# Performance work log

Hardware: AMD Instinct MI355X
Metric: run time of the kernel (lower is better)

## Reference

```python
import jax, jax.numpy as jnp
import numpy as np

TEMPERATURE = 0.5
NEG_FILL = -9000000000000000.0


def setup_inputs() -> dict:
    key = jax.random.key(0)
    z = jax.random.normal(key, (16384, 128), dtype=jnp.float32)
    return {"z": z}


def reference(z) -> jnp.ndarray:
    n2 = z.shape[0]  # 2N
    # L2 normalize rows (eps matches torch F.normalize default 1e-12)
    norm = jnp.maximum(jnp.linalg.norm(z, axis=1, keepdims=True), 1e-12)
    zn = z / norm
    # (2N, 2N) cosine similarity scaled by temperature
    sim = jnp.matmul(zn, zn.T) / TEMPERATURE
    # mask self-similarity on the diagonal
    idx = jnp.arange(n2)
    sim = jnp.where(idx[:, None] == idx[None, :], NEG_FILL, sim)
    # positive pair of row i is i^1 (2i <-> 2i+1)
    pos_indices = idx ^ 1
    pos_sim = sim[idx, pos_indices]
    loss = -pos_sim + jax.scipy.special.logsumexp(sim, axis=1)
    return jnp.mean(loss)
```

## Files before the change

### kernel.cpp

```cpp
#include <hip/hip_runtime.h>
#include <hip/hip_bf16.h>

#define N2 16384
#define D  128
#define PANEL 32768
#define C1   2.88539008177792681472f
#define SQC1 1.69864360258810896f
#define LN2  0.69314718055994530942f

typedef __bf16 bf16x8 __attribute__((ext_vector_type(8)));
typedef float  f32x4  __attribute__((ext_vector_type(4)));

#if __has_builtin(__builtin_amdgcn_exp2f)
#define EXP2(x) __builtin_amdgcn_exp2f(x)
#else
#define EXP2(x) exp2f(x)
#endif

__device__ __forceinline__ unsigned short f2bf(float f) {
    union { float f; unsigned u; } v; v.f = f;
    unsigned r = v.u + 0x7fffu + ((v.u >> 16) & 1u);
    return (unsigned short)(r >> 16);
}

__device__ __forceinline__ void stage_panel(const char* __restrict__ g,
                                            char* lds, int tid) {
    const int wid = tid >> 6, lane = tid & 63;
    #pragma unroll
    for (int i = 0; i < 8; ++i) {
        int off = (wid << 13) + (i << 10) + (lane << 4);
        int src = off ^ (((off >> 8) & 7) << 4);
        __builtin_amdgcn_global_load_lds(
            (const __attribute__((address_space(1))) unsigned*)(g + src),
            (__attribute__((address_space(3))) unsigned*)(lds + (wid << 13) + (i << 10)),
            16, 0, 0);
    }
}

__global__ void k_norm(const float* __restrict__ z, unsigned short* __restrict__ zn) {
    int row  = blockIdx.x * 4 + (threadIdx.x >> 6);
    int lane = threadIdx.x & 63;
    const float2 v = ((const float2*)(z + (size_t)row * D))[lane];
    float ss = v.x * v.x + v.y * v.y;
    #pragma unroll
    for (int m = 1; m < 64; m <<= 1) ss += __shfl_xor(ss, m);
    float inv = SQC1 / fmaxf(sqrtf(ss), 1e-12f);
    ushort2 o; o.x = f2bf(v.x * inv); o.y = f2bf(v.y * inv);
    ((ushort2*)(zn + (size_t)row * D))[lane] = o;
}

__global__ __launch_bounds__(256, 2)
void k_sim(const unsigned short* __restrict__ zn, float* __restrict__ rowsum) {
    __shared__ unsigned short ls[2][PANEL / 2];
    char* ls0 = (char*)&ls[0][0];
    char* ls1 = (char*)&ls[1][0];

    const int tileI = blockIdx.y;
    const int sBase = blockIdx.x * 16;
    const int nt = (blockIdx.x == 3 && tileI < 64) ? 17 : 16;
    const int tid  = threadIdx.x;
    const int lane = tid & 63, wid = tid >> 6;
    const int wr = wid >> 1, wc = wid & 1;
    const int l16 = lane & 15, lg = lane >> 4;
    const char* znb = (const char*)zn;
    const f32x4 ZERO = {0.f, 0.f, 0.f, 0.f};

    stage_panel(znb + (size_t)tileI * PANEL, ls0, tid);
    stage_panel(znb + (size_t)((tileI + sBase) & 127) * PANEL, ls1, tid);
    asm volatile("s_waitcnt vmcnt(8)" ::: "memory");
    __builtin_amdgcn_s_barrier();

    bf16x8 af[4][4];
    #pragma unroll
    for (int kk = 0; kk < 4; ++kk)
        #pragma unroll
        for (int m = 0; m < 4; ++m) {
            int row = wr * 64 + m * 16 + l16;
            int d = row * 256 + kk * 64 + lg * 16;
            af[kk][m] = *(const bf16x8*)(ls0 + (d ^ ((row & 7) << 4)));
        }
    asm volatile("s_waitcnt lgkmcnt(0)" ::: "memory");
    __builtin_amdgcn_s_barrier();

    float rs[4][4];
    #pragma unroll
    for (int m = 0; m < 4; ++m)
        #pragma unroll
        for (int r = 0; r < 4; ++r) rs[m][r] = 0.f;

    for (int t = 0; t < nt; ++t) {
        const int s  = sBase + t;
        const int jt = (tileI + s) & 127;
        char* rbuf = (t & 1) ? ls0 : ls1;
        char* sbuf = (t & 1) ? ls1 : ls0;
        if (t < nt - 1) {
            stage_panel(znb + (size_t)((tileI + s + 1) & 127) * PANEL, sbuf, tid);
            asm volatile("s_waitcnt vmcnt(8)" ::: "memory");
        } else {
            asm volatile("s_waitcnt vmcnt(0)" ::: "memory");
        }
        __builtin_amdgcn_s_barrier();

        bf16x8 bfr[4][4];
        #pragma unroll
        for (int kk = 0; kk < 4; ++kk)
            #pragma unroll
            for (int n = 0; n < 4; ++n) {
                int row = wc * 64 + n * 16 + l16;
                int d = row * 256 + kk * 64 + lg * 16;
                bfr[kk][n] = *(const bf16x8*)(rbuf + (d ^ ((row & 7) << 4)));
            }
        asm volatile("s_waitcnt lgkmcnt(0)" ::: "memory");
        __builtin_amdgcn_s_barrier();

        f32x4 acc[4][4];
        #pragma unroll
        for (int m = 0; m < 4; ++m)
            #pragma unroll
            for (int n = 0; n < 4; ++n)
                acc[m][n] = __builtin_amdgcn_mfma_f32_16x16x32_bf16(af[0][m], bfr[0][n], ZERO, 0, 0, 0);
        #pragma unroll
        for (int kk = 1; kk < 4; ++kk)
            #pragma unroll
            for (int m = 0; m < 4; ++m)
                #pragma unroll
                for (int n = 0; n < 4; ++n)
                    acc[m][n] = __builtin_amdgcn_mfma_f32_16x16x32_bf16(af[kk][m], bfr[kk][n], acc[m][n], 0, 0, 0);

        if (s == 0) {
            #pragma unroll
            for (int m = 0; m < 4; ++m)
                #pragma unroll
                for (int r = 0; r < 4; ++r) {
                    int li = wr * 64 + m * 16 + lg * 4 + r;
                    float a = 0.f;
                    #pragma unroll
                    for (int n = 0; n < 4; ++n) {
                        int lj = wc * 64 + n * 16 + l16;
                        float e = EXP2(acc[m][n][r]);
                        a += (li == lj) ? 0.f : e;
                    }
                    rs[m][r] += a;
                }
        } else {
            float cs[4] = {0.f, 0.f, 0.f, 0.f};
            #pragma unroll
            for (int m = 0; m < 4; ++m)
                #pragma unroll
                for (int r = 0; r < 4; ++r) {
                    float a = 0.f;
                    #pragma unroll
                    for (int n = 0; n < 4; ++n) {
                        float e = EXP2(acc[m][n][r]);
                        a += e;
                        cs[n] += e;
                    }
                    rs[m][r] += a;
                }
            #pragma unroll
            for (int n = 0; n < 4; ++n) {
                float v = cs[n];
                v += __shfl_xor(v, 16);
                v += __shfl_xor(v, 32);
                if (lg == 0)
                    atomicAdd(&rowsum[jt * 128 + wc * 64 + n * 16 + l16], v);
            }
        }
    }

    #pragma unroll
    for (int m = 0; m < 4; ++m)
        #pragma unroll
        for (int r = 0; r < 4; ++r) {
            float v = rs[m][r];
            v += __shfl_xor(v, 1);
            v += __shfl_xor(v, 2);
            v += __shfl_xor(v, 4);
            v += __shfl_xor(v, 8);
            if (l16 == 0)
                atomicAdd(&rowsum[tileI * 128 + wr * 64 + m * 16 + lg * 4 + r], v);
        }
}

__global__ void k_loss_reduce(const unsigned short* __restrict__ zn,
                              const float* __restrict__ rowsum,
                              float* __restrict__ out) {
    const int tid = threadIdx.x + blockIdx.x * 256;
    float p = 0.f;
    const bf16x8* v8 = (const bf16x8*)zn;
    for (int v = tid; v < N2 * D / 8; v += 64 * 256) {
        bf16x8 a = v8[v];
        bf16x8 b = v8[v ^ 16];
        #pragma unroll
        for (int e = 0; e < 8; ++e) p += (float)a[e] * (float)b[e];
    }
    float part = logf(rowsum[tid]) - LN2 * p;

    __shared__ float sm[4];
    #pragma unroll
    for (int m = 1; m < 64; m <<= 1) part += __shfl_xor(part, m);
    if ((threadIdx.x & 63) == 0) sm[threadIdx.x >> 6] = part;
    __syncthreads();
    if (threadIdx.x == 0)
        atomicAdd(out, (sm[0] + sm[1] + sm[2] + sm[3]) * (1.0f / (float)N2));
}

extern "C" void kernel_launch(void* const* d_in, const int* in_sizes, int n_in,
                              void* d_out, int out_size, void* d_ws, size_t ws_size,
                              hipStream_t stream) {
    const float* z = (const float*)d_in[0];
    float* out = (float*)d_out;

    unsigned short* zn = (unsigned short*)d_ws;
    float* rowsum = (float*)((char*)d_ws + (size_t)N2 * D * 2);

    hipMemsetAsync(rowsum, 0, N2 * sizeof(float), stream);
    hipMemsetAsync(out, 0, sizeof(float), stream);
    k_norm<<<N2 / 4, 256, 0, stream>>>(z, zn);
    dim3 grid(4, 128);
    k_sim<<<grid, 256, 0, stream>>>(zn, rowsum);
    k_loss_reduce<<<64, 256, 0, stream>>>(zn, rowsum, out);
}
```

Before: 68.50 us.

## Stream half-panels with smaller LDS, raise occupancy, fold memsets into norm kernel

The similarity kernel now stages half-panels of 64 rows into a 32KB LDS double buffer instead of full 128-row panels, which halves the B-fragment registers and accumulators per step. It raises launch bounds to three blocks per CU and widens the grid to six column chunks of 11 panel-steps, so more wavefronts can hide latency and the work spreads more evenly across CUs. The two memsets are removed and their zeroing moved into the normalization kernel, saving separate launches. The cost is twice as many barriers and pipeline steps per panel, more atomics per unit of work, and a serialized first panel load.

```diff
diff --git a/kernel.cpp b/kernel.cpp
--- a/kernel.cpp
+++ b/kernel.cpp
@@ -4,7 +4,7 @@
 #define N2 16384
 #define D  128
 #define PANEL 32768
-#define C1   2.88539008177792681472f
+#define HALFP 16384
 #define SQC1 1.69864360258810896f
 #define LN2  0.69314718055994530942f
 
@@ -37,7 +37,24 @@
     }
 }
 
-__global__ void k_norm(const float* __restrict__ z, unsigned short* __restrict__ zn) {
+__device__ __forceinline__ void stage_half(const char* __restrict__ g,
+                                           char* lds, int tid) {
+    const int wid = tid >> 6, lane = tid & 63;
+    #pragma unroll
+    for (int i = 0; i < 4; ++i) {
+        int off = (wid << 12) + (i << 10) + (lane << 4);
+        int src = off ^ (((off >> 8) & 7) << 4);
+        __builtin_amdgcn_global_load_lds(
+            (const __attribute__((address_space(1))) unsigned*)(g + src),
+            (__attribute__((address_space(3))) unsigned*)(lds + (wid << 12) + (i << 10)),
+            16, 0, 0);
+    }
+}
+
+__global__ void k_norm(const float* __restrict__ z, unsigned short* __restrict__ zn,
+                       float* __restrict__ rowsum, float* __restrict__ out) {
+    if (blockIdx.x < 64) rowsum[blockIdx.x * 256 + threadIdx.x] = 0.f;
+    if (blockIdx.x == 64 && threadIdx.x == 0) out[0] = 0.f;
     int row  = blockIdx.x * 4 + (threadIdx.x >> 6);
     int lane = threadIdx.x & 63;
     const float2 v = ((const float2*)(z + (size_t)row * D))[lane];
@@ -49,15 +66,17 @@
     ((ushort2*)(zn + (size_t)row * D))[lane] = o;
 }
 
-__global__ __launch_bounds__(256, 2)
+__global__ __launch_bounds__(256, 3)
 void k_sim(const unsigned short* __restrict__ zn, float* __restrict__ rowsum) {
-    __shared__ unsigned short ls[2][PANEL / 2];
-    char* ls0 = (char*)&ls[0][0];
-    char* ls1 = (char*)&ls[1][0];
-
+    __shared__ char ls[PANEL];
+    char* ls0 = ls;
+    char* ls1 = ls + HALFP;
     const int tileI = blockIdx.y;
-    const int sBase = blockIdx.x * 16;
-    const int nt = (blockIdx.x == 3 && tileI < 64) ? 17 : 16;
+    const int c = blockIdx.x;
+    const int sLo = c * 11;
+    const int sHi = (c < 5) ? (sLo + 11) : ((tileI < 64) ? 65 : 64);
+    const int Q = (sHi - sLo) * 2;
+
     const int tid  = threadIdx.x;
     const int lane = tid & 63, wid = tid >> 6;
     const int wr = wid >> 1, wc = wid & 1;
@@ -66,8 +85,7 @@
     const f32x4 ZERO = {0.f, 0.f, 0.f, 0.f};
 
     stage_panel(znb + (size_t)tileI * PANEL, ls0, tid);
-    stage_panel(znb + (size_t)((tileI + sBase) & 127) * PANEL, ls1, tid);
-    asm volatile("s_waitcnt vmcnt(8)" ::: "memory");
+    asm volatile("s_waitcnt vmcnt(0)" ::: "memory");
     __builtin_amdgcn_s_barrier();
 
     bf16x8 af[4][4];
@@ -82,49 +100,55 @@
     asm volatile("s_waitcnt lgkmcnt(0)" ::: "memory");
     __builtin_amdgcn_s_barrier();
 
+    stage_half(znb + (size_t)((tileI + sLo) & 127) * PANEL, ls0, tid);
+
     float rs[4][4];
     #pragma unroll
     for (int m = 0; m < 4; ++m)
         #pragma unroll
         for (int r = 0; r < 4; ++r) rs[m][r] = 0.f;
 
-    for (int t = 0; t < nt; ++t) {
-        const int s  = sBase + t;
+    for (int q = 0; q < Q; ++q) {
+        const int s  = sLo + (q >> 1);
+        const int h  = q & 1;
         const int jt = (tileI + s) & 127;
-        char* rbuf = (t & 1) ? ls0 : ls1;
-        char* sbuf = (t & 1) ? ls1 : ls0;
-        if (t < nt - 1) {
-            stage_panel(znb + (size_t)((tileI + s + 1) & 127) * PANEL, sbuf, tid);
-            asm volatile("s_waitcnt vmcnt(8)" ::: "memory");
+        char* rbuf = (q & 1) ? ls1 : ls0;
+        char* sbuf = (q & 1) ? ls0 : ls1;
+        if (q + 1 < Q) {
+            const int s1 = sLo + ((q + 1) >> 1);
+            const int h1 = (q + 1) & 1;
+            stage_half(znb + (size_t)((tileI + s1) & 127) * PANEL + h1 * HALFP,
+                       sbuf, tid);
+            asm volatile("s_waitcnt vmcnt(4)" ::: "memory");
         } else {
             asm volatile("s_waitcnt vmcnt(0)" ::: "memory");
         }
         __builtin_amdgcn_s_barrier();
 
-        bf16x8 bfr[4][4];
+        bf16x8 bfr[4][2];
         #pragma unroll
         for (int kk = 0; kk < 4; ++kk)
             #pragma unroll
-            for (int n = 0; n < 4; ++n) {
-                int row = wc * 64 + n * 16 + l16;
+            for (int n = 0; n < 2; ++n) {
+                int row = wc * 32 + n * 16 + l16;
                 int d = row * 256 + kk * 64 + lg * 16;
                 bfr[kk][n] = *(const bf16x8*)(rbuf + (d ^ ((row & 7) << 4)));
             }
         asm volatile("s_waitcnt lgkmcnt(0)" ::: "memory");
         __builtin_amdgcn_s_barrier();
 
-        f32x4 acc[4][4];
+        f32x4 acc[4][2];
         #pragma unroll
         for (int m = 0; m < 4; ++m)
             #pragma unroll
-            for (int n = 0; n < 4; ++n)
+            for (int n = 0; n < 2; ++n)
                 acc[m][n] = __builtin_amdgcn_mfma_f32_16x16x32_bf16(af[0][m], bfr[0][n], ZERO, 0, 0, 0);
         #pragma unroll
         for (int kk = 1; kk < 4; ++kk)
             #pragma unroll
             for (int m = 0; m < 4; ++m)
                 #pragma unroll
-                for (int n = 0; n < 4; ++n)
+                for (int n = 0; n < 2; ++n)
                     acc[m][n] = __builtin_amdgcn_mfma_f32_16x16x32_bf16(af[kk][m], bfr[kk][n], acc[m][n], 0, 0, 0);
 
         if (s == 0) {
@@ -135,35 +159,31 @@
                     int li = wr * 64 + m * 16 + lg * 4 + r;
                     float a = 0.f;
                     #pragma unroll
-                    for (int n = 0; n < 4; ++n) {
-                        int lj = wc * 64 + n * 16 + l16;
+                    for (int n = 0; n < 2; ++n) {
+                        int lj = h * 64 + wc * 32 + n * 16 + l16;
                         float e = EXP2(acc[m][n][r]);
                         a += (li == lj) ? 0.f : e;
                     }
                     rs[m][r] += a;
                 }
         } else {
-            float cs[4] = {0.f, 0.f, 0.f, 0.f};
+            float cs0 = 0.f, cs1 = 0.f;
             #pragma unroll
             for (int m = 0; m < 4; ++m)
                 #pragma unroll
                 for (int r = 0; r < 4; ++r) {
-                    float a = 0.f;
-                    #pragma unroll
-                    for (int n = 0; n < 4; ++n) {
-                        float e = EXP2(acc[m][n][r]);
-                        a += e;
-                        cs[n] += e;
-                    }
-                    rs[m][r] += a;
+                    float e0 = EXP2(acc[m][0][r]);
+                    float e1 = EXP2(acc[m][1][r]);
+                    rs[m][r] += e0 + e1;
+                    cs0 += e0; cs1 += e1;
                 }
-            #pragma unroll
-            for (int n = 0; n < 4; ++n) {
-                float v = cs[n];
-                v += __shfl_xor(v, 16);
-                v += __shfl_xor(v, 32);
-                if (lg == 0)
-                    atomicAdd(&rowsum[jt * 128 + wc * 64 + n * 16 + l16], v);
+            float v0 = cs0 + __shfl_xor(cs0, 16);
+            v0 += __shfl_xor(v0, 32);
+            float v1 = cs1 + __shfl_xor(cs1, 16);
+            v1 += __shfl_xor(v1, 32);
+            if (lg == 0) {
+                atomicAdd(&rowsum[jt * 128 + h * 64 + wc * 32 + l16], v0);
+                atomicAdd(&rowsum[jt * 128 + h * 64 + wc * 32 + 16 + l16], v1);
             }
         }
     }
@@ -214,10 +234,8 @@
     unsigned short* zn = (unsigned short*)d_ws;
     float* rowsum = (float*)((char*)d_ws + (size_t)N2 * D * 2);
 
-    hipMemsetAsync(rowsum, 0, N2 * sizeof(float), stream);
-    hipMemsetAsync(out, 0, sizeof(float), stream);
-    k_norm<<<N2 / 4, 256, 0, stream>>>(z, zn);
-    dim3 grid(4, 128);
+    k_norm<<<N2 / 4 , 256, 0, stream>>>(z, zn, rowsum, out);
+    dim3 grid(6, 128);
     k_sim<<<grid, 256, 0, stream>>>(zn, rowsum);
     k_loss_reduce<<<64, 256, 0, stream>>>(zn, rowsum, out);
 }
```

After: 69.89 us. +2.0%, slower.

## Drop LDS staging; per-wave 64x64 tiles loaded directly from global

Applied to the files above, without the earlier changes.

Rewrites the similarity kernel so each wave independently handles a 64-row tile against a chunk of 64-column tiles, loading both operands straight from global memory into registers instead of staging 128-row panels through double-buffered LDS with block barriers. It also folds the two memsets into the normalization kernel and raises wave priority around the MFMA block. This removes LDS traffic and barrier stalls and gives more independent work units. In exchange there is less operand reuse per block, so more global/L2 traffic and more atomics onto the row sums, since tiles are smaller.

```diff
diff --git a/kernel.cpp b/kernel.cpp
--- a/kernel.cpp
+++ b/kernel.cpp
@@ -3,8 +3,6 @@
 
 #define N2 16384
 #define D  128
-#define PANEL 32768
-#define C1   2.88539008177792681472f
 #define SQC1 1.69864360258810896f
 #define LN2  0.69314718055994530942f
 
@@ -23,21 +21,10 @@
     return (unsigned short)(r >> 16);
 }
 
-__device__ __forceinline__ void stage_panel(const char* __restrict__ g,
-                                            char* lds, int tid) {
-    const int wid = tid >> 6, lane = tid & 63;
-    #pragma unroll
-    for (int i = 0; i < 8; ++i) {
-        int off = (wid << 13) + (i << 10) + (lane << 4);
-        int src = off ^ (((off >> 8) & 7) << 4);
-        __builtin_amdgcn_global_load_lds(
-            (const __attribute__((address_space(1))) unsigned*)(g + src),
-            (__attribute__((address_space(3))) unsigned*)(lds + (wid << 13) + (i << 10)),
-            16, 0, 0);
-    }
-}
-
-__global__ void k_norm(const float* __restrict__ z, unsigned short* __restrict__ zn) {
+__global__ void k_norm(const float* __restrict__ z, unsigned short* __restrict__ zn,
+                       float* __restrict__ rowsum, float* __restrict__ out) {
+    if (blockIdx.x < 64) rowsum[blockIdx.x * 256 + threadIdx.x] = 0.f;
+    if (blockIdx.x == 64 && threadIdx.x == 0) out[0] = 0.f;
     int row  = blockIdx.x * 4 + (threadIdx.x >> 6);
     int lane = threadIdx.x & 63;
     const float2 v = ((const float2*)(z + (size_t)row * D))[lane];
@@ -51,36 +38,27 @@
 
 __global__ __launch_bounds__(256, 2)
 void k_sim(const unsigned short* __restrict__ zn, float* __restrict__ rowsum) {
-    __shared__ unsigned short ls[2][PANEL / 2];
-    char* ls0 = (char*)&ls[0][0];
-    char* ls1 = (char*)&ls[1][0];
-
-    const int tileI = blockIdx.y;
-    const int sBase = blockIdx.x * 16;
-    const int nt = (blockIdx.x == 3 && tileI < 64) ? 17 : 16;
-    const int tid  = threadIdx.x;
-    const int lane = tid & 63, wid = tid >> 6;
-    const int wr = wid >> 1, wc = wid & 1;
+    const int wid = threadIdx.x >> 6, lane = threadIdx.x & 63;
+    const int job = blockIdx.x * 4 + wid;
+    const int ti = job >> 3;
+    const int chunk = job & 7;
+    const int sLo = chunk * 16;
+    const int nt = (chunk == 7 && ti < 128) ? 17 : 16;
     const int l16 = lane & 15, lg = lane >> 4;
     const char* znb = (const char*)zn;
     const f32x4 ZERO = {0.f, 0.f, 0.f, 0.f};
 
-    stage_panel(znb + (size_t)tileI * PANEL, ls0, tid);
-    stage_panel(znb + (size_t)((tileI + sBase) & 127) * PANEL, ls1, tid);
-    asm volatile("s_waitcnt vmcnt(8)" ::: "memory");
-    __builtin_amdgcn_s_barrier();
+    const int laneoff = l16 * 256 + lg * 16;
 
     bf16x8 af[4][4];
-    #pragma unroll
-    for (int kk = 0; kk < 4; ++kk)
+    {
+        const char* ab = znb + (size_t)ti * 16384 + laneoff;
         #pragma unroll
-        for (int m = 0; m < 4; ++m) {
-            int row = wr * 64 + m * 16 + l16;
-            int d = row * 256 + kk * 64 + lg * 16;
-            af[kk][m] = *(const bf16x8*)(ls0 + (d ^ ((row & 7) << 4)));
-        }
-    asm volatile("s_waitcnt lgkmcnt(0)" ::: "memory");
-    __builtin_amdgcn_s_barrier();
+        for (int kk = 0; kk < 4; ++kk)
+            #pragma unroll
+            for (int m = 0; m < 4; ++m)
+                af[kk][m] = *(const bf16x8*)(ab + m * 4096 + kk * 64);
+    }
 
     float rs[4][4];
     #pragma unroll
@@ -89,31 +67,19 @@
         for (int r = 0; r < 4; ++r) rs[m][r] = 0.f;
 
     for (int t = 0; t < nt; ++t) {
-        const int s  = sBase + t;
-        const int jt = (tileI + s) & 127;
-        char* rbuf = (t & 1) ? ls0 : ls1;
-        char* sbuf = (t & 1) ? ls1 : ls0;
-        if (t < nt - 1) {
-            stage_panel(znb + (size_t)((tileI + s + 1) & 127) * PANEL, sbuf, tid);
-            asm volatile("s_waitcnt vmcnt(8)" ::: "memory");
-        } else {
-            asm volatile("s_waitcnt vmcnt(0)" ::: "memory");
-        }
-        __builtin_amdgcn_s_barrier();
+        const int s  = sLo + t;
+        const int jt = (ti + s) & 255;
+        const char* bb = znb + (size_t)jt * 16384 + laneoff;
 
         bf16x8 bfr[4][4];
         #pragma unroll
         for (int kk = 0; kk < 4; ++kk)
             #pragma unroll
-            for (int n = 0; n < 4; ++n) {
-                int row = wc * 64 + n * 16 + l16;
-                int d = row * 256 + kk * 64 + lg * 16;
-                bfr[kk][n] = *(const bf16x8*)(rbuf + (d ^ ((row & 7) << 4)));
-            }
-        asm volatile("s_waitcnt lgkmcnt(0)" ::: "memory");
-        __builtin_amdgcn_s_barrier();
+            for (int n = 0; n < 4; ++n)
+                bfr[kk][n] = *(const bf16x8*)(bb + n * 4096 + kk * 64);
 
         f32x4 acc[4][4];
+        __builtin_amdgcn_s_setprio(1);
         #pragma unroll
         for (int m = 0; m < 4; ++m)
             #pragma unroll
@@ -126,17 +92,18 @@
                 #pragma unroll
                 for (int n = 0; n < 4; ++n)
                     acc[m][n] = __builtin_amdgcn_mfma_f32_16x16x32_bf16(af[kk][m], bfr[kk][n], acc[m][n], 0, 0, 0);
+        __builtin_amdgcn_s_setprio(0);
 
         if (s == 0) {
             #pragma unroll
             for (int m = 0; m < 4; ++m)
                 #pragma unroll
                 for (int r = 0; r < 4; ++r) {
-                    int li = wr * 64 + m * 16 + lg * 4 + r;
+                    int li = m * 16 + lg * 4 + r;
                     float a = 0.f;
                     #pragma unroll
                     for (int n = 0; n < 4; ++n) {
-                        int lj = wc * 64 + n * 16 + l16;
+                        int lj = n * 16 + l16;
                         float e = EXP2(acc[m][n][r]);
                         a += (li == lj) ? 0.f : e;
                     }
@@ -163,7 +130,7 @@
                 v += __shfl_xor(v, 16);
                 v += __shfl_xor(v, 32);
                 if (lg == 0)
-                    atomicAdd(&rowsum[jt * 128 + wc * 64 + n * 16 + l16], v);
+                    atomicAdd(&rowsum[jt * 64 + n * 16 + l16], v);
             }
         }
     }
@@ -178,7 +145,7 @@
             v += __shfl_xor(v, 4);
             v += __shfl_xor(v, 8);
             if (l16 == 0)
-                atomicAdd(&rowsum[tileI * 128 + wr * 64 + m * 16 + lg * 4 + r], v);
+                atomicAdd(&rowsum[ti * 64 + m * 16 + lg * 4 + r], v);
         }
 }
 
@@ -214,10 +181,7 @@
     unsigned short* zn = (unsigned short*)d_ws;
     float* rowsum = (float*)((char*)d_ws + (size_t)N2 * D * 2);
 
-    hipMemsetAsync(rowsum, 0, N2 * sizeof(float), stream);
-    hipMemsetAsync(out, 0, sizeof(float), stream);
-    k_norm<<<N2 / 4, 256, 0, stream>>>(z, zn);
-    dim3 grid(4, 128);
-    k_sim<<<grid, 256, 0, stream>>>(zn, rowsum);
+    k_norm<<<N2 / 4, 256, 0, stream>>>(z, zn, rowsum, out);
+    k_sim<<<512, 256, 0, stream>>>(zn, rowsum);
     k_loss_reduce<<<64, 256, 0, stream>>>(zn, rowsum, out);
 }
```

Result: slower. 86.65 us (+26.5%).
